# Optimization experiments

Hardware: AMD Instinct MI355X
Metric: run time of the kernel (lower is better)

The kernel has to match this reference:

```python
import jax, jax.numpy as jnp
import numpy as np

LAMBDA1 = 1.0  # init kwarg lambda1
N, D = 4000000, 16


def setup_inputs() -> dict:
    key = jax.random.key(0)
    k1, k2 = jax.random.split(key)
    y1 = jax.random.normal(k1, (N, D), dtype=jnp.float32)
    yinds = jax.random.randint(k2, (N,), 0, N, dtype=jnp.int64)
    return {"y1": y1, "yinds": yinds}


def reference(y1, yinds):
    # mfld_type == 'Sn': project each point onto the unit sphere (row-wise L2 norm),
    # vectorized over the batch instead of the original per-point Python loop.
    norms = jnp.linalg.norm(y1, axis=1, keepdims=True)  # [N, 1]
    ws = y1 / norms                                      # [N, D]
    # nn.MSELoss default reduction='mean' over all elements, scaled by lambda1
    loss = LAMBDA1 * jnp.mean((ws - y1) ** 2)
    return loss
```

## Files before the change

kernel.cpp:

```cpp
#include <hip/hip_runtime.h>


#define GRID1 2048

__global__ __launch_bounds__(256) void mll_pass1_kernel(
    const float* __restrict__ y1, double* __restrict__ partials, int total4) {
    const int tid    = blockIdx.x * blockDim.x + threadIdx.x;
    const int stride = gridDim.x * blockDim.x;

    float psum = 0.0f;
    const float4* __restrict__ y4 = reinterpret_cast<const float4*>(y1);
    for (int idx = tid; idx < total4; idx += stride) {
        const float4 v = y4[idx];
        const float local = v.x * v.x + v.y * v.y + v.z * v.z + v.w * v.w;
        float row = local;
        row += __shfl_xor(row, 1);
        row += __shfl_xor(row, 2);
        const float c = 1.0f / sqrtf(row) - 1.0f;
        psum += local * c * c;
    }

    #pragma unroll
    for (int off = 32; off > 0; off >>= 1)
        psum += __shfl_xor(psum, off);

    __shared__ float wsum[4];
    const int lane = threadIdx.x & 63;
    const int wave = threadIdx.x >> 6;
    if (lane == 0) wsum[wave] = psum;
    __syncthreads();
    if (threadIdx.x == 0) {
        partials[blockIdx.x] = (double)(wsum[0] + wsum[1] + wsum[2] + wsum[3]);
    }
}

__global__ __launch_bounds__(256) void mll_pass2_kernel(
    const double* __restrict__ partials, float* __restrict__ out,
    int n_partials, double inv_m) {
    double s = 0.0;
    for (int i = threadIdx.x; i < n_partials; i += 256) s += partials[i];
    #pragma unroll
    for (int off = 32; off > 0; off >>= 1)
        s += __shfl_xor(s, off);
    __shared__ double wsum[4];
    const int lane = threadIdx.x & 63;
    const int wave = threadIdx.x >> 6;
    if (lane == 0) wsum[wave] = s;
    __syncthreads();
    if (threadIdx.x == 0) {
        out[0] = (float)((wsum[0] + wsum[1] + wsum[2] + wsum[3]) * inv_m);
    }
}

extern "C" void kernel_launch(void* const* d_in, const int* in_sizes, int n_in,
                              void* d_out, int out_size, void* d_ws, size_t ws_size,
                              hipStream_t stream) {
    const float* y1 = (const float*)d_in[0];
    const int total  = in_sizes[0];
    const int total4 = total / 4;
    double* partials = (double*)d_ws;

    mll_pass1_kernel<<<GRID1, 256, 0, stream>>>(y1, partials, total4);
    mll_pass2_kernel<<<1, 256, 0, stream>>>(partials, (float*)d_out,
                                            GRID1, 1.0 / (double)total);
}
```

Baseline: 342.7 us.

## Fuse two-pass reduction with last-block atomic counter and unroll loads by four

```diff
diff --git a/kernel.cpp b/kernel.cpp
--- a/kernel.cpp
+++ b/kernel.cpp
@@ -3,21 +3,37 @@
 
 #define GRID1 2048
 
-__global__ __launch_bounds__(256) void mll_pass1_kernel(
-    const float* __restrict__ y1, double* __restrict__ partials, int total4) {
+__device__ __forceinline__ float quad_term(float4 v) {
+    const float local = v.x * v.x + v.y * v.y + v.z * v.z + v.w * v.w;
+    float row = local;
+    row += __shfl_xor(row, 1);
+    row += __shfl_xor(row, 2);
+    const float c = 1.0f / sqrtf(row) - 1.0f;
+    return local * c * c;
+}
+
+__global__ __launch_bounds__(256) void mll_fused_kernel(
+    const float* __restrict__ y1, unsigned int* __restrict__ counter,
+    double* __restrict__ partials, float* __restrict__ out,
+    int total4, double inv_m) {
     const int tid    = blockIdx.x * blockDim.x + threadIdx.x;
     const int stride = gridDim.x * blockDim.x;
 
+    const float4* __restrict__ y4 = reinterpret_cast<const float4*>(y1);
     float psum = 0.0f;
-    const float4* __restrict__ y4 = reinterpret_cast<const float4*>(y1);
-    for (int idx = tid; idx < total4; idx += stride) {
-        const float4 v = y4[idx];
-        const float local = v.x * v.x + v.y * v.y + v.z * v.z + v.w * v.w;
-        float row = local;
-        row += __shfl_xor(row, 1);
-        row += __shfl_xor(row, 2);
-        const float c = 1.0f / sqrtf(row) - 1.0f;
-        psum += local * c * c;
+    int idx = tid;
+    for (; idx + 3 * stride < total4; idx += 4 * stride) {
+        const float4 v0 = y4[idx];
+        const float4 v1 = y4[idx + stride];
+        const float4 v2 = y4[idx + 2 * stride];
+        const float4 v3 = y4[idx + 3 * stride];
+        psum += quad_term(v0);
+        psum += quad_term(v1);
+        psum += quad_term(v2);
+        psum += quad_term(v3);
+    }
+    for (; idx < total4; idx += stride) {
+        psum += quad_term(y4[idx]);
     }
 
     #pragma unroll
@@ -29,26 +45,28 @@
     const int wave = threadIdx.x >> 6;
     if (lane == 0) wsum[wave] = psum;
     __syncthreads();
+
+    __shared__ bool amLast;
     if (threadIdx.x == 0) {
         partials[blockIdx.x] = (double)(wsum[0] + wsum[1] + wsum[2] + wsum[3]);
+        __threadfence();
+        const unsigned int old = atomicAdd(counter, 1u);
+        amLast = (old == (unsigned int)(gridDim.x - 1));
     }
-}
+    __syncthreads();
 
-__global__ __launch_bounds__(256) void mll_pass2_kernel(
-    const double* __restrict__ partials, float* __restrict__ out,
-    int n_partials, double inv_m) {
-    double s = 0.0;
-    for (int i = threadIdx.x; i < n_partials; i += 256) s += partials[i];
-    #pragma unroll
-    for (int off = 32; off > 0; off >>= 1)
-        s += __shfl_xor(s, off);
-    __shared__ double wsum[4];
-    const int lane = threadIdx.x & 63;
-    const int wave = threadIdx.x >> 6;
-    if (lane == 0) wsum[wave] = s;
-    __syncthreads();
-    if (threadIdx.x == 0) {
-        out[0] = (float)((wsum[0] + wsum[1] + wsum[2] + wsum[3]) * inv_m);
+    if (amLast) {
+        __threadfence();
+        double s = 0.0;
+        for (int i = threadIdx.x; i < GRID1; i += 256) s += partials[i];
+        #pragma unroll
+        for (int off = 32; off > 0; off >>= 1)
+            s += __shfl_xor(s, off);
+        __shared__ double dsum[4];
+        if (lane == 0) dsum[wave] = s;
+        __syncthreads();
+        if (threadIdx.x == 0)
+            out[0] = (float)((dsum[0] + dsum[1] + dsum[2] + dsum[3]) * inv_m);
     }
 }
 
@@ -58,9 +76,11 @@
     const float* y1 = (const float*)d_in[0];
     const int total  = in_sizes[0];
     const int total4 = total / 4;
-    double* partials = (double*)d_ws;
 
-    mll_pass1_kernel<<<GRID1, 256, 0, stream>>>(y1, partials, total4);
-    mll_pass2_kernel<<<1, 256, 0, stream>>>(partials, (float*)d_out,
-                                            GRID1, 1.0 / (double)total);
+    unsigned int* counter = (unsigned int*)d_ws;
+    double* partials = (double*)((char*)d_ws + 8);
+
+    hipMemsetAsync(counter, 0, sizeof(unsigned int), stream);
+    mll_fused_kernel<<<GRID1, 256, 0, stream>>>(
+        y1, counter, partials, (float*)d_out, total4, 1.0 / (double)total);
 }
```

Measured after the change: 450.8 us. 1.32x slower.

## Software-prefetch next float4 and use DPP lane swaps and rsqrt in row reduction

Applied to the files above, without the earlier changes.

```diff
diff --git a/kernel.cpp b/kernel.cpp
--- a/kernel.cpp
+++ b/kernel.cpp
@@ -3,21 +3,39 @@
 
 #define GRID1 2048
 
+__device__ __forceinline__ float dpp_add_xor1(float x) {
+    int j = __builtin_amdgcn_mov_dpp(__float_as_int(x), 0xB1, 0xF, 0xF, true);
+    return x + __int_as_float(j);
+}
+__device__ __forceinline__ float dpp_add_xor2(float x) {
+    int j = __builtin_amdgcn_mov_dpp(__float_as_int(x), 0x4E, 0xF, 0xF, true);
+    return x + __int_as_float(j);
+}
+
+__device__ __forceinline__ float row_term(float4 v) {
+    const float local = v.x * v.x + v.y * v.y + v.z * v.z + v.w * v.w;
+    const float S = dpp_add_xor2(dpp_add_xor1(local));
+    const float t = rsqrtf(S) - 1.0f;
+    return local * (t * t);
+}
+
 __global__ __launch_bounds__(256) void mll_pass1_kernel(
     const float* __restrict__ y1, double* __restrict__ partials, int total4) {
     const int tid    = blockIdx.x * blockDim.x + threadIdx.x;
-    const int stride = gridDim.x * blockDim.x;
+    const int stride = GRID1 * 256;
 
+    const float4* __restrict__ y4 = reinterpret_cast<const float4*>(y1);
     float psum = 0.0f;
-    const float4* __restrict__ y4 = reinterpret_cast<const float4*>(y1);
-    for (int idx = tid; idx < total4; idx += stride) {
-        const float4 v = y4[idx];
-        const float local = v.x * v.x + v.y * v.y + v.z * v.z + v.w * v.w;
-        float row = local;
-        row += __shfl_xor(row, 1);
-        row += __shfl_xor(row, 2);
-        const float c = 1.0f / sqrtf(row) - 1.0f;
-        psum += local * c * c;
+    int idx = tid;
+    if (idx < total4) {
+        float4 cur = y4[idx];
+        idx += stride;
+        for (; idx < total4; idx += stride) {
+            const float4 nxt = y4[idx];
+            psum += row_term(cur);
+            cur = nxt;
+        }
+        psum += row_term(cur);
     }
 
     #pragma unroll
@@ -29,9 +47,8 @@
     const int wave = threadIdx.x >> 6;
     if (lane == 0) wsum[wave] = psum;
     __syncthreads();
-    if (threadIdx.x == 0) {
+    if (threadIdx.x == 0)
         partials[blockIdx.x] = (double)(wsum[0] + wsum[1] + wsum[2] + wsum[3]);
-    }
 }
 
 __global__ __launch_bounds__(256) void mll_pass2_kernel(
@@ -47,9 +64,8 @@
     const int wave = threadIdx.x >> 6;
     if (lane == 0) wsum[wave] = s;
     __syncthreads();
-    if (threadIdx.x == 0) {
+    if (threadIdx.x == 0)
         out[0] = (float)((wsum[0] + wsum[1] + wsum[2] + wsum[3]) * inv_m);
-    }
 }
 
 extern "C" void kernel_launch(void* const* d_in, const int* in_sizes, int n_in,
```

Measured after the change: 342.9 us. About the same (+0.1%).
